# Kernel optimization log

Hardware: AMD Instinct MI355X
Metric: run time of the kernel (lower is better)

The kernel has to match this reference:

```python
import jax, jax.numpy as jnp
import numpy as np

N_NODES = 50000
N_EDGES = 1_600_000
IN_DIM = 6
EMB = 64
EDGE_DIM = 1
L = 4
BN_EPS = 1e-5


def _bn_relu(x, gamma, beta):
    # BatchNorm1d in training mode: biased batch stats over the row dim.
    mu = jnp.mean(x, axis=0)
    var = jnp.var(x, axis=0)
    xhat = (x - mu) * jax.lax.rsqrt(var + BN_EPS)
    return jax.nn.relu(xhat * gamma + beta)


def setup_inputs() -> dict:
    key = jax.random.key(0)
    ks = jax.random.split(key, 32)
    s = 0.1
    inp = {
        "x": jax.random.normal(ks[0], (N_NODES, IN_DIM), jnp.float32),
        "edge_index": jax.random.randint(ks[1], (2, N_EDGES), 0, N_NODES),
        "edge_attr": jax.random.normal(ks[2], (N_EDGES, EDGE_DIM), jnp.float32),
        "lin_in_W": jax.random.normal(ks[3], (IN_DIM, EMB)) * s,
        "lin_in_b": jnp.zeros((EMB,)),
        # per-layer stacked params, leading dim L
        "msg_W1": jax.random.normal(ks[4], (L, 2 * EMB + EDGE_DIM, EMB)) * s,
        "msg_b1": jnp.zeros((L, EMB)),
        "msg_g1": jnp.ones((L, EMB)),
        "msg_be1": jnp.zeros((L, EMB)),
        "msg_W2": jax.random.normal(ks[5], (L, EMB, EMB)) * s,
        "msg_b2": jnp.zeros((L, EMB)),
        "msg_g2": jnp.ones((L, EMB)),
        "msg_be2": jnp.zeros((L, EMB)),
        "upd_W1": jax.random.normal(ks[6], (L, 2 * EMB, EMB)) * s,
        "upd_b1": jnp.zeros((L, EMB)),
        "upd_g1": jnp.ones((L, EMB)),
        "upd_be1": jnp.zeros((L, EMB)),
        "upd_W2": jax.random.normal(ks[7], (L, EMB, EMB)) * s,
        "upd_b2": jnp.zeros((L, EMB)),
        "upd_g2": jnp.ones((L, EMB)),
        "upd_be2": jnp.zeros((L, EMB)),
        "pred_W": jax.random.normal(ks[8], (EMB, 1)) * s,
        "pred_b": jnp.zeros((1,)),
    }
    return inp


def reference(x, edge_index, edge_attr, lin_in_W, lin_in_b,
              msg_W1, msg_b1, msg_g1, msg_be1, msg_W2, msg_b2, msg_g2, msg_be2,
              upd_W1, upd_b1, upd_g1, upd_be1, upd_W2, upd_b2, upd_g2, upd_be2,
              pred_W, pred_b):
    n = x.shape[0]
    src = edge_index[0]  # j (source)
    dst = edge_index[1]  # i (target / aggregation index)

    h = x @ lin_in_W + lin_in_b  # (n, d)
    for l in range(L):
        h_i = h[dst]                              # (e, d) destination feats
        h_j = h[src]                              # (e, d) source feats
        m = jnp.concatenate([h_i, h_j, edge_attr], axis=-1)  # (e, 2d+de)
        m = _bn_relu(m @ msg_W1[l] + msg_b1[l], msg_g1[l], msg_be1[l])
        m = _bn_relu(m @ msg_W2[l] + msg_b2[l], msg_g2[l], msg_be2[l])
        aggr = jax.ops.segment_sum(m, dst, num_segments=n)   # (n, d)
        u = jnp.concatenate([h, aggr], axis=-1)              # (n, 2d)
        u = _bn_relu(u @ upd_W1[l] + upd_b1[l], upd_g1[l], upd_be1[l])
        u = _bn_relu(u @ upd_W2[l] + upd_b2[l], upd_g2[l], upd_be2[l])
        h = h + u  # residual
    out = h @ pred_W + pred_b
    return out.reshape(-1)
```

## Files before the change

### kernel.cpp

```cpp
#include <hip/hip_runtime.h>
#include <hip/hip_bf16.h>


#define BN_EPS 1e-5f
#define NSH 128
#define TPB 4
#define LYS 72
#define LW1S 168
#define LW2S 68
#define ASW 66

typedef __attribute__((ext_vector_type(4))) short short4v;
typedef __attribute__((ext_vector_type(8))) short short8;
typedef __attribute__((ext_vector_type(16))) float floatx16;

#define MFMA32 __builtin_amdgcn_mfma_f32_32x32x16_bf16

__device__ __forceinline__ short f2bs(float f) {
  union { float f; unsigned u; } x; x.f = f;
  unsigned r = x.u + 0x7fffu + ((x.u >> 16) & 1u);
  return (short)(r >> 16);
}
__device__ __forceinline__ short f2bs_fast(float f) {
  union { float f; unsigned u; } x; x.f = f;
  return (short)((x.u + 0x8000u) >> 16);
}
__device__ __forceinline__ float bs2f(short s) {
  union { unsigned u; float f; } x;
  x.u = ((unsigned)(unsigned short)s) << 16;
  return x.f;
}


__global__ void lin_in_kernel(const float* __restrict__ x,
                              const float* __restrict__ W,
                              const float* __restrict__ b, float* __restrict__ h,
                              short* __restrict__ hb, int N) {
  int gid = blockIdx.x * blockDim.x + threadIdx.x;
  if (gid >= N * 64) return;
  int n = gid >> 6, o = gid & 63;
  float acc = b[o];
#pragma unroll
  for (int k = 0; k < 6; ++k) acc += x[n * 6 + k] * W[k * 64 + o];
  h[gid] = acc;
  hb[gid] = f2bs(acc);
}

__global__ void deg_kernel(const int* __restrict__ ei, int* __restrict__ deg,
                           int E) {
  int gid = blockIdx.x * blockDim.x + threadIdx.x;
  if (gid < E) atomicAdd(&deg[ei[E + gid]], 1);
}

__global__ void scan_kernel(const int* __restrict__ deg, int* __restrict__ offs,
                            int N) {
  __shared__ int s[1024];
  int t = threadIdx.x;
  int chunk = (N + 1023) >> 10;
  int lo = t * chunk, hi = lo + chunk;
  if (hi > N) hi = N;
  if (lo > N) lo = N;
  int tot = 0;
  for (int i = lo; i < hi; ++i) tot += deg[i];
  s[t] = tot;
  __syncthreads();
  for (int off = 1; off < 1024; off <<= 1) {
    int v = (t >= off) ? s[t - off] : 0;
    __syncthreads();
    s[t] += v;
    __syncthreads();
  }
  int run = s[t] - tot;
  for (int i = lo; i < hi; ++i) {
    offs[i] = run;
    run += deg[i];
  }
}

__global__ void fill_kernel(const int* __restrict__ ei,
                            const int* __restrict__ offs, int* __restrict__ cnt,
                            int* __restrict__ sorted, int E) {
  int gid = blockIdx.x * blockDim.x + threadIdx.x;
  if (gid >= E) return;
  int d = ei[E + gid];
  int pos = offs[d] + atomicAdd(&cnt[d], 1);
  sorted[pos] = gid;
}

__global__ void gather_edges_kernel(const int* __restrict__ ei,
                                    const int* __restrict__ sorted,
                                    const float* __restrict__ ea,
                                    int* __restrict__ dd, int* __restrict__ ds,
                                    short* __restrict__ es, int E, int Epad) {
  int i = blockIdx.x * 256 + threadIdx.x;
  if (i >= Epad) return;
  if (i < E) {
    int e = sorted[i];
    dd[i] = ei[E + e];
    ds[i] = ei[e];
    es[i] = f2bs(ea[e]);
  } else {
    dd[i] = -1;
    ds[i] = 0;
    es[i] = 0;
  }
}

__global__ void pack_w1_kernel(const float* __restrict__ W,
                               short* __restrict__ Wt, int L_) {
  int i = blockIdx.x * 256 + threadIdx.x;
  if (i >= L_ * 64 * 160) return;
  int k = i % 160, n = (i / 160) % 64, l = i / (160 * 64);
  Wt[i] = (k < 129) ? f2bs(W[((size_t)l * 129 + k) * 64 + n]) : (short)0;
}

__global__ void pack_w2_kernel(const float* __restrict__ W,
                               short* __restrict__ Wt, int L_) {
  int i = blockIdx.x * 256 + threadIdx.x;
  if (i >= L_ * 64 * 64) return;
  int k = i % 64, n = (i / 64) % 64, l = i / 4096;
  Wt[i] = f2bs(W[((size_t)l * 64 + k) * 64 + n]);
}

__global__ void bn_finalize_kernel(const float* __restrict__ shards,
                                   const float* __restrict__ gamma,
                                   const float* __restrict__ beta, float cnt,
                                   float* __restrict__ ac) {
  int o = threadIdx.x;
  float s = 0.f, q = 0.f;
  for (int i = 0; i < NSH; ++i) {
    s += shards[i * 128 + o];
    q += shards[i * 128 + 64 + o];
  }
  float mu = s / cnt;
  float var = fmaxf(q / cnt - mu * mu, 0.f);
  float r = rsqrtf(var + BN_EPS);
  float g = gamma[o];
  ac[o] = g * r;
  ac[64 + o] = beta[o] - mu * g * r;
}

__global__ void bn_finalize_pack1(const float* __restrict__ shards,
                                  const float* __restrict__ gamma,
                                  const float* __restrict__ beta, float cnt,
                                  const float* __restrict__ W,
                                  const float* __restrict__ b,
                                  short* __restrict__ Wt,
                                  float* __restrict__ bs) {
  __shared__ float sa[64];
  int t = threadIdx.x;
  if (t < 64) {
    float s = 0.f, q = 0.f;
    for (int i = 0; i < NSH; ++i) {
      s += shards[i * 128 + t];
      q += shards[i * 128 + 64 + t];
    }
    float mu = s / cnt;
    float var = fmaxf(q / cnt - mu * mu, 0.f);
    float r = rsqrtf(var + BN_EPS);
    float a = gamma[t] * r;
    float c = beta[t] - mu * a;
    sa[t] = a;
    if (blockIdx.x == 0) bs[t] = a * b[t] + c;
  }
  __syncthreads();
  int i = blockIdx.x * 256 + t;
  if (i < 64 * 160) {
    int k = i % 160, n = i / 160;
    Wt[i] = (k < 129) ? f2bs(W[k * 64 + n] * sa[n]) : (short)0;
  }
}

__global__ void bn_finalize_pack2(const float* __restrict__ shards,
                                  const float* __restrict__ gamma,
                                  const float* __restrict__ beta, float cnt,
                                  const float* __restrict__ W,
                                  const float* __restrict__ b,
                                  short* __restrict__ Wt,
                                  float* __restrict__ bs) {
  __shared__ float sa[64];
  int t = threadIdx.x;
  if (t < 64) {
    float s = 0.f, q = 0.f;
    for (int i = 0; i < NSH; ++i) {
      s += shards[i * 128 + t];
      q += shards[i * 128 + 64 + t];
    }
    float mu = s / cnt;
    float var = fmaxf(q / cnt - mu * mu, 0.f);
    float r = rsqrtf(var + BN_EPS);
    float a = gamma[t] * r;
    float c = beta[t] - mu * a;
    sa[t] = a;
    if (blockIdx.x == 0) bs[t] = a * b[t] + c;
  }
  __syncthreads();
  int i = blockIdx.x * 256 + t;
  if (i < 64 * 64) {
    int k = i % 64, n = i / 64;
    Wt[i] = f2bs(W[k * 64 + n] * sa[n]);
  }
}


__device__ __forceinline__ void stage_w1(const short* __restrict__ Wt,
                                         short* Lw, int t) {
#pragma unroll
  for (int i = 0; i < 5; ++i) {
    int c = t + i * 256;
    int col = c / 20, ch = c % 20;
    *(short8*)&Lw[col * LW1S + ch * 8] = *(const short8*)&Wt[col * 160 + ch * 8];
  }
}
__device__ __forceinline__ void stage_w2(const short* __restrict__ Wt,
                                         short* Lw, int t) {
#pragma unroll
  for (int i = 0; i < 2; ++i) {
    int c = t + i * 256;
    int col = c >> 3, ch = c & 7;
    *(short8*)&Lw[col * LW2S + ch * 8] = *(const short8*)&Wt[col * 64 + ch * 8];
  }
}

__device__ __forceinline__ void gemm1_32(const short* __restrict__ hbf,
                                         const short* Lw1,
                                         const float* __restrict__ bias, int d,
                                         int sx, short eav, int me, int hl,
                                         floatx16 acc[2]) {
  const short* hd = hbf + (size_t)d * 64 + hl * 8;
  const short* hs = hbf + (size_t)sx * 64 + hl * 8;
  short8 A[8];
#pragma unroll
  for (int kc = 0; kc < 4; ++kc) A[kc] = *(const short8*)(hd + kc * 16);
#pragma unroll
  for (int kc = 0; kc < 4; ++kc) A[4 + kc] = *(const short8*)(hs + kc * 16);
  short8 a8 = {0, 0, 0, 0, 0, 0, 0, 0};
  if (hl == 0) a8[0] = eav;
#pragma unroll
  for (int nt = 0; nt < 2; ++nt) {
    int col = nt * 32 + me;
    float bv = bias[col];
    floatx16 a;
#pragma unroll
    for (int r = 0; r < 16; ++r) a[r] = bv;
    const short* wp = Lw1 + col * LW1S + hl * 8;
#pragma unroll
    for (int kc = 0; kc < 8; ++kc) {
      short8 B = *(const short8*)(wp + kc * 16);
      a = MFMA32(A[kc], B, a, 0, 0, 0);
    }
    short8 B8 = *(const short8*)(wp + 128);
    a = MFMA32(a8, B8, a, 0, 0, 0);
    acc[nt] = a;
  }
}

__device__ __forceinline__ void load_frag(const short* __restrict__ hbf, int d,
                                          int sx, int hl, short8 Bf[8]) {
  int dc = d < 0 ? 0 : d;
  const short* hd = hbf + (size_t)dc * 64 + hl * 8;
  const short* hs = hbf + (size_t)sx * 64 + hl * 8;
#pragma unroll
  for (int kc = 0; kc < 4; ++kc) Bf[kc] = *(const short8*)(hd + kc * 16);
#pragma unroll
  for (int kc = 0; kc < 4; ++kc) Bf[4 + kc] = *(const short8*)(hs + kc * 16);
}

__device__ __forceinline__ void gemm1T_mfma(const short* Lw1,
                                            const short8 Bf[8], short eav,
                                            int me, int hl, floatx16 acc[2]) {
  short8 b8 = {0, 0, 0, 0, 0, 0, 0, 0};
  if (hl == 0) b8[0] = eav;
#pragma unroll
  for (int nt = 0; nt < 2; ++nt) {
    floatx16 a;
#pragma unroll
    for (int r = 0; r < 16; ++r) a[r] = 0.f;
    const short* wp = Lw1 + (nt * 32 + me) * LW1S + hl * 8;
#pragma unroll
    for (int kc = 0; kc < 8; ++kc) {
      short8 A = *(const short8*)(wp + kc * 16);
      a = MFMA32(A, Bf[kc], a, 0, 0, 0);
    }
    short8 A8 = *(const short8*)(wp + 128);
    a = MFMA32(A8, b8, a, 0, 0, 0);
    acc[nt] = a;
  }
}

__device__ __forceinline__ void gemm1T_32(const short* __restrict__ hbf,
                                          const short* Lw1, int d, int sx,
                                          short eav, int me, int hl,
                                          floatx16 acc[2]) {
  short8 Bf[8];
  load_frag(hbf, d, sx, hl, Bf);
  gemm1T_mfma(Lw1, Bf, eav, me, hl, acc);
}

__device__ __forceinline__ void write_z(short* Lz, const floatx16 acc[2],
                                        const float b1v[2][16], int w, int me,
                                        int hl) {
#pragma unroll
  for (int nt = 0; nt < 2; ++nt)
#pragma unroll
    for (int g4 = 0; g4 < 4; ++g4) {
      int n1b = nt * 32 + 8 * g4 + 4 * hl;
      short4v pk;
#pragma unroll
      for (int j = 0; j < 4; ++j) {
        int r = g4 * 4 + j;
        pk[j] = f2bs_fast(fmaxf(acc[nt][r] + b1v[nt][r], 0.f));
      }
      *(short4v*)&Lz[(w * 32 + me) * LYS + n1b] = pk;
    }
}

__device__ __forceinline__ void gemm2_32(const short* Lz, const short* Lw2,
                                         const float* __restrict__ bias, int w,
                                         int me, int hl, floatx16 acc[2]) {
  short8 Z[4];
  const short* zp = &Lz[(w * 32 + me) * LYS + hl * 8];
#pragma unroll
  for (int kc = 0; kc < 4; ++kc) Z[kc] = *(const short8*)(zp + kc * 16);
#pragma unroll
  for (int nt = 0; nt < 2; ++nt) {
    int col = nt * 32 + me;
    float bv = bias[col];
    floatx16 a;
#pragma unroll
    for (int r = 0; r < 16; ++r) a[r] = bv;
    const short* wp = Lw2 + col * LW2S + hl * 8;
#pragma unroll
    for (int kc = 0; kc < 4; ++kc) {
      short8 B = *(const short8*)(wp + kc * 16);
      a = MFMA32(Z[kc], B, a, 0, 0, 0);
    }
    acc[nt] = a;
  }
}

__device__ __forceinline__ void stats32_acc(const floatx16 acc[2], int idx0,
                                            int w, int hl, int E, bool full,
                                            float sa[2], float qa[2]) {
#pragma unroll
  for (int nt = 0; nt < 2; ++nt) {
    float s = 0.f, q = 0.f;
#pragma unroll
    for (int r = 0; r < 16; ++r) {
      float v = acc[nt][r];
      if (!full) {
        int row = (r & 3) + 8 * (r >> 2) + 4 * hl;
        if (idx0 + w * 32 + row >= E) v = 0.f;
      }
      s += v;
      q += v * v;
    }
    s += __shfl_down(s, 32, 64);
    q += __shfl_down(q, 32, 64);
    sa[nt] += s;
    qa[nt] += q;
  }
}

__device__ __forceinline__ void stats_epilogue(float sred[4][128],
                                               const float sa[2],
                                               const float qa[2], int w,
                                               int lane, int t,
                                               float* __restrict__ stat,
                                               int shard) {
  if (lane < 32) {
#pragma unroll
    for (int nt = 0; nt < 2; ++nt) {
      sred[w][nt * 32 + lane] = sa[nt];
      sred[w][64 + nt * 32 + lane] = qa[nt];
    }
  }
  __syncthreads();
  if (t < 128) {
    float v = sred[0][t] + sred[1][t] + sred[2][t] + sred[3][t];
    atomicAdd(&stat[(size_t)shard * 128 + t], v);
  }
}


__global__ __launch_bounds__(256) void edge_pass_a(
    const short* __restrict__ hbf, const short* __restrict__ Wt1,
    const float* __restrict__ b1, const int* __restrict__ dd,
    const int* __restrict__ dsr, const short* __restrict__ es,
    float* __restrict__ stat, int E, int Epad) {
  __shared__ __align__(16) short Lw1[64 * LW1S];
  __shared__ float sred[4][128];
  int t = threadIdx.x;
  stage_w1(Wt1, Lw1, t);
  __syncthreads();
  int w = t >> 6, lane = t & 63, me = lane & 31, hl = lane >> 5;
  float sa[2] = {0.f, 0.f}, qa[2] = {0.f, 0.f};
  for (int it = 0; it < TPB; ++it) {
    int idx0 = (blockIdx.x * TPB + it) * 128;
    if (idx0 >= Epad) break;
    int eg = idx0 + w * 32 + me;
    int d = dd[eg];
    int dc = d < 0 ? 0 : d;
    int sx = dsr[eg];
    short eav = es[eg];
    floatx16 acc[2];
    gemm1_32(hbf, Lw1, b1, dc, sx, eav, me, hl, acc);
    stats32_acc(acc, idx0, w, hl, E, idx0 + 128 <= E, sa, qa);
  }
  stats_epilogue(sred, sa, qa, w, lane, t, stat, blockIdx.x & (NSH - 1));
}

__global__ __launch_bounds__(256) void edge_pass_b(
    const short* __restrict__ hbf, const short* __restrict__ Wt1s,
    const float* __restrict__ b1s, const int* __restrict__ dd,
    const int* __restrict__ dsr, const short* __restrict__ es,
    const short* __restrict__ Wt2, const float* __restrict__ b2,
    float* __restrict__ stat, int E, int Epad) {
  __shared__ __align__(16) short Lw1[64 * LW1S];
  __shared__ __align__(16) short Lw2[64 * LW2S];
  __shared__ __align__(16) short Lz[128 * LYS];
  __shared__ float sred[4][128];
  int t = threadIdx.x;
  stage_w1(Wt1s, Lw1, t);
  stage_w2(Wt2, Lw2, t);
  __syncthreads();
  int w = t >> 6, lane = t & 63, me = lane & 31, hl = lane >> 5;
  float b1v[2][16];
#pragma unroll
  for (int nt = 0; nt < 2; ++nt)
#pragma unroll
    for (int r = 0; r < 16; ++r)
      b1v[nt][r] = b1s[nt * 32 + (r & 3) + 8 * (r >> 2) + 4 * hl];
  float sa[2] = {0.f, 0.f}, qa[2] = {0.f, 0.f};
  for (int it = 0; it < TPB; ++it) {
    int idx0 = (blockIdx.x * TPB + it) * 128;
    if (idx0 >= Epad) break;
    int eg = idx0 + w * 32 + me;
    int d = dd[eg];
    int dc = d < 0 ? 0 : d;
    int sx = dsr[eg];
    short eav = es[eg];
    floatx16 acc[2];
    gemm1T_32(hbf, Lw1, dc, sx, eav, me, hl, acc);
    write_z(Lz, acc, b1v, w, me, hl);
    floatx16 acc2[2];
    gemm2_32(Lz, Lw2, b2, w, me, hl, acc2);
    stats32_acc(acc2, idx0, w, hl, E, idx0 + 128 <= E, sa, qa);
  }
  stats_epilogue(sred, sa, qa, w, lane, t, stat, blockIdx.x & (NSH - 1));
}

__global__ __launch_bounds__(256) void edge_pass_c(
    const short* __restrict__ hbf, const short* __restrict__ Wt1s,
    const float* __restrict__ b1s, const int* __restrict__ dd,
    const int* __restrict__ dsr, const short* __restrict__ es,
    const short* __restrict__ Wt2s, const float* __restrict__ b2s,
    float* __restrict__ aggr, int E, int Epad) {
  __shared__ __align__(16) short Lw1[64 * LW1S];
  __shared__ __align__(16) short Lw2[64 * LW2S];
  __shared__ __align__(16) short Lz[128 * LYS];
  __shared__ int sdstw[4][32];
  int t = threadIdx.x;
  stage_w1(Wt1s, Lw1, t);
  stage_w2(Wt2s, Lw2, t);
  int w = t >> 6, lane = t & 63, me = lane & 31, hl = lane >> 5;
  const int base0 = blockIdx.x * TPB * 128;
  int d_c, sx_c, d_n, sx_n;
  short eav_c, eav_n;
  {
    int eg = base0 + w * 32 + me;
    d_c = dd[eg];
    sx_c = dsr[eg];
    eav_c = es[eg];
    int i1 = base0 + 128;
    if (i1 < Epad) {
      d_n = dd[i1 + w * 32 + me];
      sx_n = dsr[i1 + w * 32 + me];
      eav_n = es[i1 + w * 32 + me];
    } else {
      d_n = -1;
      sx_n = 0;
      eav_n = 0;
    }
  }
  short8 Bf_c[8], Bf_n[8];
  load_frag(hbf, d_c, sx_c, hl, Bf_c);
  __syncthreads();
  float b1v[2][16];
#pragma unroll
  for (int nt = 0; nt < 2; ++nt)
#pragma unroll
    for (int r = 0; r < 16; ++r)
      b1v[nt][r] = b1s[nt * 32 + (r & 3) + 8 * (r >> 2) + 4 * hl];
#pragma unroll
  for (int it = 0; it < TPB; ++it) {
    int idx0 = base0 + it * 128;
    if (idx0 < Epad) {
      bool nv = (idx0 + 128) < Epad;
      if (nv) load_frag(hbf, d_n, sx_n, hl, Bf_n);
      int d_2 = -1, sx_2 = 0;
      short eav_2 = 0;
      int i2 = idx0 + 256;
      if (it + 2 < TPB && i2 < Epad) {
        d_2 = dd[i2 + w * 32 + me];
        sx_2 = dsr[i2 + w * 32 + me];
        eav_2 = es[i2 + w * 32 + me];
      }
      if (lane < 32) sdstw[w][lane] = d_c;
      floatx16 acc[2];
      gemm1T_mfma(Lw1, Bf_c, eav_c, me, hl, acc);
      write_z(Lz, acc, b1v, w, me, hl);
      floatx16 acc2[2];
      gemm2_32(Lz, Lw2, b2s, w, me, hl, acc2);
      float s0 = 0.f, s1 = 0.f;
      int d2 = sdstw[w][4 * hl];
#pragma unroll
      for (int g4 = 0; g4 < 4; ++g4) {
#pragma unroll
        for (int j = 0; j < 4; ++j) {
          int r = g4 * 4 + j;
          s0 += fmaxf(acc2[0][r], 0.f);
          s1 += fmaxf(acc2[1][r], 0.f);
          int offn;
          if (j == 3)
            offn = (g4 == 3) ? -1 : 8 * (g4 + 1) + 4 * hl;
          else
            offn = 8 * g4 + 4 * hl + j + 1;
          int dn = (offn < 0) ? -2 : sdstw[w][offn];
          if (d2 != dn) {
            if (d2 >= 0) {
              atomicAdd(&aggr[(size_t)d2 * 64 + me], s0);
              atomicAdd(&aggr[(size_t)d2 * 64 + me + 32], s1);
            }
            s0 = 0.f;
            s1 = 0.f;
          }
          d2 = dn;
        }
      }
#pragma unroll
      for (int kc = 0; kc < 8; ++kc) Bf_c[kc] = Bf_n[kc];
      d_c = d_n;
      sx_c = sx_n;
      eav_c = eav_n;
      d_n = d_2;
      sx_n = sx_2;
      eav_n = eav_2;
    }
  }
}


__device__ __forceinline__ void gemm_r2c8(const float* __restrict__ As,
                                          const float* __restrict__ W, int K,
                                          int rg, int cg, float acc[2][8]) {
  const float* ap = As + rg * 2;
  const float* wp = W + cg * 8;
#pragma unroll 4
  for (int k = 0; k < K; ++k) {
    float2 a = *(const float2*)&ap[k * ASW];
    float4 w0 = *(const float4*)&wp[k * 64];
    float4 w1 = *(const float4*)&wp[k * 64 + 4];
    float wv[8] = {w0.x, w0.y, w0.z, w0.w, w1.x, w1.y, w1.z, w1.w};
#pragma unroll
    for (int j = 0; j < 8; ++j) {
      acc[0][j] += a.x * wv[j];
      acc[1][j] += a.y * wv[j];
    }
  }
}

__device__ __forceinline__ void stats_r2c8(const float acc[2][8],
                                           float* __restrict__ shard, int t,
                                           int cg) {
  float s[8], q[8];
#pragma unroll
  for (int j = 0; j < 8; ++j) {
    s[j] = acc[0][j] + acc[1][j];
    q[j] = acc[0][j] * acc[0][j] + acc[1][j] * acc[1][j];
  }
#pragma unroll
  for (int off = 32; off >= 8; off >>= 1) {
#pragma unroll
    for (int j = 0; j < 8; ++j) {
      s[j] += __shfl_down(s[j], off, 64);
      q[j] += __shfl_down(q[j], off, 64);
    }
  }
  if (((t & 63) >> 3) == 0) {
#pragma unroll
    for (int j = 0; j < 8; ++j) {
      atomicAdd(&shard[cg * 8 + j], s[j]);
      atomicAdd(&shard[64 + cg * 8 + j], q[j]);
    }
  }
}

__global__ __launch_bounds__(256) void node_gemm1_v3(
    const float* __restrict__ h, const float* __restrict__ aggr,
    const float* __restrict__ W, const float* __restrict__ b,
    float* __restrict__ u1, float* __restrict__ stat, int N) {
  __shared__ __align__(16) float As[128 * ASW];
  int n0 = blockIdx.x * 64;
  int t = threadIdx.x;
  int c = t & 63, g = t >> 6;
  for (int n = g; n < 64; n += 4) {
    int idx = n0 + n;
    bool v = idx < N;
    As[c * ASW + n] = v ? h[(size_t)idx * 64 + c] : 0.f;
    As[(64 + c) * ASW + n] = v ? aggr[(size_t)idx * 64 + c] : 0.f;
  }
  __syncthreads();
  int rg = t >> 3, cg = t & 7;
  float acc[2][8];
#pragma unroll
  for (int i = 0; i < 2; ++i)
#pragma unroll
    for (int j = 0; j < 8; ++j) acc[i][j] = b[cg * 8 + j];
  gemm_r2c8(As, W, 128, rg, cg, acc);
#pragma unroll
  for (int i = 0; i < 2; ++i) {
    int idx = n0 + rg * 2 + i;
    if (idx < N) {
      *(float4*)&u1[(size_t)idx * 64 + cg * 8] =
          make_float4(acc[i][0], acc[i][1], acc[i][2], acc[i][3]);
      *(float4*)&u1[(size_t)idx * 64 + cg * 8 + 4] =
          make_float4(acc[i][4], acc[i][5], acc[i][6], acc[i][7]);
    } else {
#pragma unroll
      for (int j = 0; j < 8; ++j) acc[i][j] = 0.f;
    }
  }
  stats_r2c8(acc, stat + (size_t)(blockIdx.x & (NSH - 1)) * 128, t, cg);
}

__global__ __launch_bounds__(256) void node_gemm2_v3(
    const float* __restrict__ u1, const float* __restrict__ ac,
    const float* __restrict__ W, const float* __restrict__ b,
    float* __restrict__ u2, float* __restrict__ stat, int N) {
  __shared__ __align__(16) float As[64 * ASW];
  int n0 = blockIdx.x * 64;
  int t = threadIdx.x;
  int c = t & 63, g = t >> 6;
  float a1 = ac[c], c1 = ac[64 + c];
  for (int n = g; n < 64; n += 4) {
    int idx = n0 + n;
    bool v = idx < N;
    As[c * ASW + n] = v ? fmaxf(u1[(size_t)idx * 64 + c] * a1 + c1, 0.f) : 0.f;
  }
  __syncthreads();
  int rg = t >> 3, cg = t & 7;
  float acc[2][8];
#pragma unroll
  for (int i = 0; i < 2; ++i)
#pragma unroll
    for (int j = 0; j < 8; ++j) acc[i][j] = b[cg * 8 + j];
  gemm_r2c8(As, W, 64, rg, cg, acc);
#pragma unroll
  for (int i = 0; i < 2; ++i) {
    int idx = n0 + rg * 2 + i;
    if (idx < N) {
      *(float4*)&u2[(size_t)idx * 64 + cg * 8] =
          make_float4(acc[i][0], acc[i][1], acc[i][2], acc[i][3]);
      *(float4*)&u2[(size_t)idx * 64 + cg * 8 + 4] =
          make_float4(acc[i][4], acc[i][5], acc[i][6], acc[i][7]);
    } else {
#pragma unroll
      for (int j = 0; j < 8; ++j) acc[i][j] = 0.f;
    }
  }
  stats_r2c8(acc, stat + (size_t)(blockIdx.x & (NSH - 1)) * 128, t, cg);
}

__global__ void residual_kernel(float* __restrict__ h, short* __restrict__ hb,
                                const float* __restrict__ u2,
                                const float* __restrict__ ac, int total) {
  int gid = blockIdx.x * blockDim.x + threadIdx.x;
  if (gid >= total) return;
  int o = gid & 63;
  float v = u2[gid] * ac[o] + ac[64 + o];
  float nv = h[gid] + fmaxf(v, 0.f);
  h[gid] = nv;
  hb[gid] = f2bs(nv);
}

__global__ void pred_kernel(const float* __restrict__ h,
                            const float* __restrict__ W,
                            const float* __restrict__ b,
                            float* __restrict__ out, int N) {
  int n = blockIdx.x * blockDim.x + threadIdx.x;
  if (n >= N) return;
  float acc = b[0];
  const float* hr = h + (size_t)n * 64;
#pragma unroll
  for (int o = 0; o < 64; ++o) acc += hr[o] * W[o];
  out[n] = acc;
}


extern "C" void kernel_launch(void* const* d_in, const int* in_sizes, int n_in,
                              void* d_out, int out_size, void* d_ws,
                              size_t ws_size, hipStream_t stream) {
  const float* x = (const float*)d_in[0];
  const int* ei = (const int*)d_in[1];
  const float* ea = (const float*)d_in[2];
  const float* lin_W = (const float*)d_in[3];
  const float* lin_b = (const float*)d_in[4];
  const float* msg_W1 = (const float*)d_in[5];
  const float* msg_b1 = (const float*)d_in[6];
  const float* msg_g1 = (const float*)d_in[7];
  const float* msg_be1 = (const float*)d_in[8];
  const float* msg_W2 = (const float*)d_in[9];
  const float* msg_b2 = (const float*)d_in[10];
  const float* msg_g2 = (const float*)d_in[11];
  const float* msg_be2 = (const float*)d_in[12];
  const float* upd_W1 = (const float*)d_in[13];
  const float* upd_b1 = (const float*)d_in[14];
  const float* upd_g1 = (const float*)d_in[15];
  const float* upd_be1 = (const float*)d_in[16];
  const float* upd_W2 = (const float*)d_in[17];
  const float* upd_b2 = (const float*)d_in[18];
  const float* upd_g2 = (const float*)d_in[19];
  const float* upd_be2 = (const float*)d_in[20];
  const float* pred_W = (const float*)d_in[21];
  const float* pred_b = (const float*)d_in[22];
  float* out = (float*)d_out;

  const int N = in_sizes[0] / 6;
  const int E = in_sizes[1] / 2;
  const int L = 4;
  const int Epad = ((E + 127) / 128) * 128;

  char* p = (char*)d_ws;
  auto alloc = [&](size_t bytes) {
    void* r = (void*)p;
    p += (bytes + 255) & ~(size_t)255;
    return r;
  };
  float* h = (float*)alloc((size_t)N * 64 * 4);
  short* hb = (short*)alloc((size_t)N * 64 * 2);
  float* aggr = (float*)alloc((size_t)N * 64 * 4);
  float* stats = (float*)alloc((size_t)4 * NSH * 128 * 4);
  float* acu1 = (float*)alloc(128 * 4);
  float* acu2 = (float*)alloc(128 * 4);
  float* b1s = (float*)alloc(64 * 4);
  float* b2s = (float*)alloc(64 * 4);
  float* u1 = (float*)alloc((size_t)N * 64 * 4);
  float* u2 = (float*)alloc((size_t)N * 64 * 4);
  int* deg = (int*)alloc((size_t)N * 4);
  int* offs = (int*)alloc((size_t)N * 4);
  int* cnt = (int*)alloc((size_t)N * 4);
  int* sorted = (int*)alloc((size_t)E * 4);
  int* dd = (int*)alloc((size_t)Epad * 4);
  int* dsr = (int*)alloc((size_t)Epad * 4);
  short* es = (short*)alloc((size_t)Epad * 2);
  short* Wt1 = (short*)alloc((size_t)L * 64 * 160 * 2);
  short* Wt2 = (short*)alloc((size_t)L * 64 * 64 * 2);
  short* Wt1s = (short*)alloc((size_t)64 * 160 * 2);
  short* Wt2s = (short*)alloc((size_t)64 * 64 * 2);

  const int B = 256;
  const size_t REG = (size_t)NSH * 128;
  int gridE256 = (E + 255) / 256;
  int NT = Epad / 128;
  int gridEdge = (NT + TPB - 1) / TPB;
  int gridM64 = (N + 63) / 64;
  int gridN64 = (N * 64 + B - 1) / B;
  int gridN = (N + B - 1) / B;

  hipMemsetAsync(deg, 0, (size_t)N * 4, stream);
  hipMemsetAsync(cnt, 0, (size_t)N * 4, stream);
  lin_in_kernel<<<gridN64, B, 0, stream>>>(x, lin_W, lin_b, h, hb, N);
  deg_kernel<<<gridE256, B, 0, stream>>>(ei, deg, E);
  scan_kernel<<<1, 1024, 0, stream>>>(deg, offs, N);
  fill_kernel<<<gridE256, B, 0, stream>>>(ei, offs, cnt, sorted, E);
  gather_edges_kernel<<<(Epad + 255) / 256, B, 0, stream>>>(ei, sorted, ea, dd,
                                                            dsr, es, E, Epad);
  pack_w1_kernel<<<(L * 64 * 160 + 255) / 256, B, 0, stream>>>(msg_W1, Wt1, L);
  pack_w2_kernel<<<(L * 64 * 64 + 255) / 256, B, 0, stream>>>(msg_W2, Wt2, L);

  for (int l = 0; l < L; ++l) {
    const short* Wt1l = Wt1 + (size_t)l * 64 * 160;
    const short* Wt2l = Wt2 + (size_t)l * 64 * 64;
    const float* U1 = upd_W1 + (size_t)l * 128 * 64;
    const float* U2 = upd_W2 + (size_t)l * 64 * 64;
    hipMemsetAsync(aggr, 0, (size_t)N * 64 * 4 + (size_t)4 * REG * 4, stream);
    edge_pass_a<<<gridEdge, 256, 0, stream>>>(hb, Wt1l, msg_b1 + l * 64, dd,
                                              dsr, es, stats, E, Epad);
    bn_finalize_pack1<<<(64 * 160 + 255) / 256, B, 0, stream>>>(
        stats, msg_g1 + l * 64, msg_be1 + l * 64, (float)E,
        msg_W1 + (size_t)l * 129 * 64, msg_b1 + l * 64, Wt1s, b1s);
    edge_pass_b<<<gridEdge, 256, 0, stream>>>(hb, Wt1s, b1s, dd, dsr, es, Wt2l,
                                              msg_b2 + l * 64, stats + REG, E,
                                              Epad);
    bn_finalize_pack2<<<(64 * 64 + 255) / 256, B, 0, stream>>>(
        stats + REG, msg_g2 + l * 64, msg_be2 + l * 64, (float)E,
        msg_W2 + (size_t)l * 64 * 64, msg_b2 + l * 64, Wt2s, b2s);
    edge_pass_c<<<gridEdge, 256, 0, stream>>>(hb, Wt1s, b1s, dd, dsr, es, Wt2s,
                                              b2s, aggr, E, Epad);
    node_gemm1_v3<<<gridM64, 256, 0, stream>>>(h, aggr, U1, upd_b1 + l * 64,
                                               u1, stats + 2 * REG, N);
    bn_finalize_kernel<<<1, 64, 0, stream>>>(stats + 2 * REG, upd_g1 + l * 64,
                                             upd_be1 + l * 64, (float)N, acu1);
    node_gemm2_v3<<<gridM64, 256, 0, stream>>>(u1, acu1, U2, upd_b2 + l * 64,
                                               u2, stats + 3 * REG, N);
    bn_finalize_kernel<<<1, 64, 0, stream>>>(stats + 3 * REG, upd_g2 + l * 64,
                                             upd_be2 + l * 64, (float)N, acu2);
    residual_kernel<<<gridN64, B, 0, stream>>>(h, hb, u2, acu2, N * 64);
  }
  pred_kernel<<<gridN, B, 0, stream>>>(h, pred_W, pred_b, out, N);
}
```

Baseline: 1.870 ms.

## Software-pipeline edge gathers in BN stats passes with register double-buffering

The two edge passes that compute batch-norm statistics now prefetch the next tile's gathered node features and the tile-after-next's edge indices into registers while the current tile's MFMAs run. The first tile's loads are issued before the weight-staging barrier, so global gather latency overlaps with LDS staging and compute. The cost is roughly double the fragment registers per thread (two sets of eight short8 fragments), which may lower occupancy. A fully unrolled loop replaces the early break.

```diff
diff --git a/kernel.cpp b/kernel.cpp
--- a/kernel.cpp
+++ b/kernel.cpp
@@ -222,39 +222,6 @@
   }
 }
 
-__device__ __forceinline__ void gemm1_32(const short* __restrict__ hbf,
-                                         const short* Lw1,
-                                         const float* __restrict__ bias, int d,
-                                         int sx, short eav, int me, int hl,
-                                         floatx16 acc[2]) {
-  const short* hd = hbf + (size_t)d * 64 + hl * 8;
-  const short* hs = hbf + (size_t)sx * 64 + hl * 8;
-  short8 A[8];
-#pragma unroll
-  for (int kc = 0; kc < 4; ++kc) A[kc] = *(const short8*)(hd + kc * 16);
-#pragma unroll
-  for (int kc = 0; kc < 4; ++kc) A[4 + kc] = *(const short8*)(hs + kc * 16);
-  short8 a8 = {0, 0, 0, 0, 0, 0, 0, 0};
-  if (hl == 0) a8[0] = eav;
-#pragma unroll
-  for (int nt = 0; nt < 2; ++nt) {
-    int col = nt * 32 + me;
-    float bv = bias[col];
-    floatx16 a;
-#pragma unroll
-    for (int r = 0; r < 16; ++r) a[r] = bv;
-    const short* wp = Lw1 + col * LW1S + hl * 8;
-#pragma unroll
-    for (int kc = 0; kc < 8; ++kc) {
-      short8 B = *(const short8*)(wp + kc * 16);
-      a = MFMA32(A[kc], B, a, 0, 0, 0);
-    }
-    short8 B8 = *(const short8*)(wp + 128);
-    a = MFMA32(a8, B8, a, 0, 0, 0);
-    acc[nt] = a;
-  }
-}
-
 __device__ __forceinline__ void load_frag(const short* __restrict__ hbf, int d,
                                           int sx, int hl, short8 Bf[8]) {
   int dc = d < 0 ? 0 : d;
@@ -266,6 +233,32 @@
   for (int kc = 0; kc < 4; ++kc) Bf[4 + kc] = *(const short8*)(hs + kc * 16);
 }
 
+__device__ __forceinline__ void gemm1_mfma_std(const short* Lw1,
+                                               const float* __restrict__ bias,
+                                               const short8 Af[8], short eav,
+                                               int me, int hl,
+                                               floatx16 acc[2]) {
+  short8 a8 = {0, 0, 0, 0, 0, 0, 0, 0};
+  if (hl == 0) a8[0] = eav;
+#pragma unroll
+  for (int nt = 0; nt < 2; ++nt) {
+    int col = nt * 32 + me;
+    float bv = bias[col];
+    floatx16 a;
+#pragma unroll
+    for (int r = 0; r < 16; ++r) a[r] = bv;
+    const short* wp = Lw1 + col * LW1S + hl * 8;
+#pragma unroll
+    for (int kc = 0; kc < 8; ++kc) {
+      short8 B = *(const short8*)(wp + kc * 16);
+      a = MFMA32(Af[kc], B, a, 0, 0, 0);
+    }
+    short8 B8 = *(const short8*)(wp + 128);
+    a = MFMA32(a8, B8, a, 0, 0, 0);
+    acc[nt] = a;
+  }
+}
+
 __device__ __forceinline__ void gemm1T_mfma(const short* Lw1,
                                             const short8 Bf[8], short eav,
                                             int me, int hl, floatx16 acc[2]) {
@@ -286,15 +279,6 @@
     a = MFMA32(A8, b8, a, 0, 0, 0);
     acc[nt] = a;
   }
-}
-
-__device__ __forceinline__ void gemm1T_32(const short* __restrict__ hbf,
-                                          const short* Lw1, int d, int sx,
-                                          short eav, int me, int hl,
-                                          floatx16 acc[2]) {
-  short8 Bf[8];
-  load_frag(hbf, d, sx, hl, Bf);
-  gemm1T_mfma(Lw1, Bf, eav, me, hl, acc);
 }
 
 __device__ __forceinline__ void write_z(short* Lz, const floatx16 acc[2],
@@ -392,20 +376,56 @@
   __shared__ float sred[4][128];
   int t = threadIdx.x;
   stage_w1(Wt1, Lw1, t);
+  int w = t >> 6, lane = t & 63, me = lane & 31, hl = lane >> 5;
+  const int base0 = blockIdx.x * TPB * 128;
+  int d_c, sx_c, d_n, sx_n;
+  short eav_c, eav_n;
+  {
+    int eg = base0 + w * 32 + me;
+    d_c = dd[eg];
+    sx_c = dsr[eg];
+    eav_c = es[eg];
+    int i1 = base0 + 128;
+    if (i1 < Epad) {
+      d_n = dd[i1 + w * 32 + me];
+      sx_n = dsr[i1 + w * 32 + me];
+      eav_n = es[i1 + w * 32 + me];
+    } else {
+      d_n = -1;
+      sx_n = 0;
+      eav_n = 0;
+    }
+  }
+  short8 Af_c[8], Af_n[8];
+  load_frag(hbf, d_c, sx_c, hl, Af_c);
   __syncthreads();
-  int w = t >> 6, lane = t & 63, me = lane & 31, hl = lane >> 5;
   float sa[2] = {0.f, 0.f}, qa[2] = {0.f, 0.f};
+#pragma unroll
   for (int it = 0; it < TPB; ++it) {
-    int idx0 = (blockIdx.x * TPB + it) * 128;
-    if (idx0 >= Epad) break;
-    int eg = idx0 + w * 32 + me;
-    int d = dd[eg];
-    int dc = d < 0 ? 0 : d;
-    int sx = dsr[eg];
-    short eav = es[eg];
-    floatx16 acc[2];
-    gemm1_32(hbf, Lw1, b1, dc, sx, eav, me, hl, acc);
-    stats32_acc(acc, idx0, w, hl, E, idx0 + 128 <= E, sa, qa);
+    int idx0 = base0 + it * 128;
+    if (idx0 < Epad) {
+      bool nv = (idx0 + 128) < Epad;
+      if (nv) load_frag(hbf, d_n, sx_n, hl, Af_n);
+      int d_2 = -1, sx_2 = 0;
+      short eav_2 = 0;
+      int i2 = idx0 + 256;
+      if (it + 2 < TPB && i2 < Epad) {
+        d_2 = dd[i2 + w * 32 + me];
+        sx_2 = dsr[i2 + w * 32 + me];
+        eav_2 = es[i2 + w * 32 + me];
+      }
+      floatx16 acc[2];
+      gemm1_mfma_std(Lw1, b1, Af_c, eav_c, me, hl, acc);
+      stats32_acc(acc, idx0, w, hl, E, idx0 + 128 <= E, sa, qa);
+#pragma unroll
+      for (int kc = 0; kc < 8; ++kc) Af_c[kc] = Af_n[kc];
+      d_c = d_n;
+      sx_c = sx_n;
+      eav_c = eav_n;
+      d_n = d_2;
+      sx_n = sx_2;
+      eav_n = eav_2;
+    }
   }
   stats_epilogue(sred, sa, qa, w, lane, t, stat, blockIdx.x & (NSH - 1));
 }
@@ -423,8 +443,29 @@
   int t = threadIdx.x;
   stage_w1(Wt1s, Lw1, t);
   stage_w2(Wt2, Lw2, t);
+  int w = t >> 6, lane = t & 63, me = lane & 31, hl = lane >> 5;
+  const int base0 = blockIdx.x * TPB * 128;
+  int d_c, sx_c, d_n, sx_n;
+  short eav_c, eav_n;
+  {
+    int eg = base0 + w * 32 + me;
+    d_c = dd[eg];
+    sx_c = dsr[eg];
+    eav_c = es[eg];
+    int i1 = base0 + 128;
+    if (i1 < Epad) {
+      d_n = dd[i1 + w * 32 + me];
+      sx_n = dsr[i1 + w * 32 + me];
+      eav_n = es[i1 + w * 32 + me];
+    } else {
+      d_n = -1;
+      sx_n = 0;
+      eav_n = 0;
+    }
+  }
+  short8 Bf_c[8], Bf_n[8];
+  load_frag(hbf, d_c, sx_c, hl, Bf_c);
   __syncthreads();
-  int w = t >> 6, lane = t & 63, me = lane & 31, hl = lane >> 5;
   float b1v[2][16];
 #pragma unroll
   for (int nt = 0; nt < 2; ++nt)
@@ -432,20 +473,35 @@
     for (int r = 0; r < 16; ++r)
       b1v[nt][r] = b1s[nt * 32 + (r & 3) + 8 * (r >> 2) + 4 * hl];
   float sa[2] = {0.f, 0.f}, qa[2] = {0.f, 0.f};
+#pragma unroll
   for (int it = 0; it < TPB; ++it) {
-    int idx0 = (blockIdx.x * TPB + it) * 128;
-    if (idx0 >= Epad) break;
-    int eg = idx0 + w * 32 + me;
-    int d = dd[eg];
-    int dc = d < 0 ? 0 : d;
-    int sx = dsr[eg];
-    short eav = es[eg];
-    floatx16 acc[2];
-    gemm1T_32(hbf, Lw1, dc, sx, eav, me, hl, acc);
-    write_z(Lz, acc, b1v, w, me, hl);
-    floatx16 acc2[2];
-    gemm2_32(Lz, Lw2, b2, w, me, hl, acc2);
-    stats32_acc(acc2, idx0, w, hl, E, idx0 + 128 <= E, sa, qa);
+    int idx0 = base0 + it * 128;
+    if (idx0 < Epad) {
+      bool nv = (idx0 + 128) < Epad;
+      if (nv) load_frag(hbf, d_n, sx_n, hl, Bf_n);
+      int d_2 = -1, sx_2 = 0;
+      short eav_2 = 0;
+      int i2 = idx0 + 256;
+      if (it + 2 < TPB && i2 < Epad) {
+        d_2 = dd[i2 + w * 32 + me];
+        sx_2 = dsr[i2 + w * 32 + me];
+        eav_2 = es[i2 + w * 32 + me];
+      }
+      floatx16 acc[2];
+      gemm1T_mfma(Lw1, Bf_c, eav_c, me, hl, acc);
+      write_z(Lz, acc, b1v, w, me, hl);
+      floatx16 acc2[2];
+      gemm2_32(Lz, Lw2, b2, w, me, hl, acc2);
+      stats32_acc(acc2, idx0, w, hl, E, idx0 + 128 <= E, sa, qa);
+#pragma unroll
+      for (int kc = 0; kc < 8; ++kc) Bf_c[kc] = Bf_n[kc];
+      d_c = d_n;
+      sx_c = sx_n;
+      eav_c = eav_n;
+      d_n = d_2;
+      sx_n = sx_2;
+      eav_n = eav_2;
+    }
   }
   stats_epilogue(sred, sa, qa, w, lane, t, stat, blockIdx.x & (NSH - 1));
 }
```

Result: slower. 1.946 ms (+4.1%).

## Hold second-layer weights in registers and move bias to LDS for occupancy

Applied to the files above, without the earlier changes.

Layer-2 message weights now stay in per-lane registers instead of an LDS tile. The first-layer bias, formerly a 32-float register array per thread, now lives in a small LDS array read as float4. The stats reduction reuses the Lz buffer instead of a separate shared array. Launch bounds request 4 blocks per CU. The aim is to free LDS and VGPRs for higher occupancy in the edge passes, at the cost of more register pressure from the weight fragments and extra LDS reads for the bias.

```diff
diff --git a/kernel.cpp b/kernel.cpp
--- a/kernel.cpp
+++ b/kernel.cpp
@@ -7,7 +7,6 @@
 #define TPB 4
 #define LYS 72
 #define LW1S 168
-#define LW2S 68
 #define ASW 66
 
 typedef __attribute__((ext_vector_type(4))) short short4v;
@@ -212,14 +211,34 @@
     *(short8*)&Lw[col * LW1S + ch * 8] = *(const short8*)&Wt[col * 160 + ch * 8];
   }
 }
-__device__ __forceinline__ void stage_w2(const short* __restrict__ Wt,
-                                         short* Lw, int t) {
-#pragma unroll
-  for (int i = 0; i < 2; ++i) {
-    int c = t + i * 256;
-    int col = c >> 3, ch = c & 7;
-    *(short8*)&Lw[col * LW2S + ch * 8] = *(const short8*)&Wt[col * 64 + ch * 8];
-  }
+
+__device__ __forceinline__ void stage_b1l(const float* __restrict__ b1s,
+                                          float* Lb1, int t) {
+  if (t < 64) {
+    int hl_ = t >> 5, rem = t & 31, nt_ = rem >> 4, r_ = rem & 15;
+    Lb1[t] = b1s[nt_ * 32 + (r_ & 3) + 8 * (r_ >> 2) + 4 * hl_];
+  }
+}
+
+__device__ __forceinline__ void load_w2_regs(const short* __restrict__ Wt2,
+                                             int me, int hl, short8 w2r[2][4]) {
+#pragma unroll
+  for (int nt = 0; nt < 2; ++nt) {
+    const short* wp = Wt2 + (nt * 32 + me) * 64 + hl * 8;
+#pragma unroll
+    for (int kc = 0; kc < 4; ++kc) w2r[nt][kc] = *(const short8*)(wp + kc * 16);
+  }
+}
+
+__device__ __forceinline__ void load_frag(const short* __restrict__ hbf, int d,
+                                          int sx, int hl, short8 Bf[8]) {
+  int dc = d < 0 ? 0 : d;
+  const short* hd = hbf + (size_t)dc * 64 + hl * 8;
+  const short* hs = hbf + (size_t)sx * 64 + hl * 8;
+#pragma unroll
+  for (int kc = 0; kc < 4; ++kc) Bf[kc] = *(const short8*)(hd + kc * 16);
+#pragma unroll
+  for (int kc = 0; kc < 4; ++kc) Bf[4 + kc] = *(const short8*)(hs + kc * 16);
 }
 
 __device__ __forceinline__ void gemm1_32(const short* __restrict__ hbf,
@@ -255,17 +274,6 @@
   }
 }
 
-__device__ __forceinline__ void load_frag(const short* __restrict__ hbf, int d,
-                                          int sx, int hl, short8 Bf[8]) {
-  int dc = d < 0 ? 0 : d;
-  const short* hd = hbf + (size_t)dc * 64 + hl * 8;
-  const short* hs = hbf + (size_t)sx * 64 + hl * 8;
-#pragma unroll
-  for (int kc = 0; kc < 4; ++kc) Bf[kc] = *(const short8*)(hd + kc * 16);
-#pragma unroll
-  for (int kc = 0; kc < 4; ++kc) Bf[4 + kc] = *(const short8*)(hs + kc * 16);
-}
-
 __device__ __forceinline__ void gemm1T_mfma(const short* Lw1,
                                             const short8 Bf[8], short eav,
                                             int me, int hl, floatx16 acc[2]) {
@@ -298,43 +306,38 @@
 }
 
 __device__ __forceinline__ void write_z(short* Lz, const floatx16 acc[2],
-                                        const float b1v[2][16], int w, int me,
+                                        const float* Lb1, int w, int me,
                                         int hl) {
 #pragma unroll
   for (int nt = 0; nt < 2; ++nt)
 #pragma unroll
     for (int g4 = 0; g4 < 4; ++g4) {
+      float4 bq = *(const float4*)&Lb1[hl * 32 + nt * 16 + 4 * g4];
       int n1b = nt * 32 + 8 * g4 + 4 * hl;
       short4v pk;
-#pragma unroll
-      for (int j = 0; j < 4; ++j) {
-        int r = g4 * 4 + j;
-        pk[j] = f2bs_fast(fmaxf(acc[nt][r] + b1v[nt][r], 0.f));
-      }
+      pk[0] = f2bs_fast(fmaxf(acc[nt][4 * g4 + 0] + bq.x, 0.f));
+      pk[1] = f2bs_fast(fmaxf(acc[nt][4 * g4 + 1] + bq.y, 0.f));
+      pk[2] = f2bs_fast(fmaxf(acc[nt][4 * g4 + 2] + bq.z, 0.f));
+      pk[3] = f2bs_fast(fmaxf(acc[nt][4 * g4 + 3] + bq.w, 0.f));
       *(short4v*)&Lz[(w * 32 + me) * LYS + n1b] = pk;
     }
 }
 
-__device__ __forceinline__ void gemm2_32(const short* Lz, const short* Lw2,
-                                         const float* __restrict__ bias, int w,
-                                         int me, int hl, floatx16 acc[2]) {
+__device__ __forceinline__ void gemm2_w2r(const short* Lz,
+                                          const short8 w2r[2][4],
+                                          const float bv2[2], int w, int me,
+                                          int hl, floatx16 acc[2]) {
   short8 Z[4];
   const short* zp = &Lz[(w * 32 + me) * LYS + hl * 8];
 #pragma unroll
   for (int kc = 0; kc < 4; ++kc) Z[kc] = *(const short8*)(zp + kc * 16);
 #pragma unroll
   for (int nt = 0; nt < 2; ++nt) {
-    int col = nt * 32 + me;
-    float bv = bias[col];
     floatx16 a;
 #pragma unroll
-    for (int r = 0; r < 16; ++r) a[r] = bv;
-    const short* wp = Lw2 + col * LW2S + hl * 8;
-#pragma unroll
-    for (int kc = 0; kc < 4; ++kc) {
-      short8 B = *(const short8*)(wp + kc * 16);
-      a = MFMA32(Z[kc], B, a, 0, 0, 0);
-    }
+    for (int r = 0; r < 16; ++r) a[r] = bv2[nt];
+#pragma unroll
+    for (int kc = 0; kc < 4; ++kc) a = MFMA32(Z[kc], w2r[nt][kc], a, 0, 0, 0);
     acc[nt] = a;
   }
 }
@@ -378,6 +381,28 @@
   __syncthreads();
   if (t < 128) {
     float v = sred[0][t] + sred[1][t] + sred[2][t] + sred[3][t];
+    atomicAdd(&stat[(size_t)shard * 128 + t], v);
+  }
+}
+
+__device__ __forceinline__ void stats_epilogue_lz(short* Lz, const float sa[2],
+                                                  const float qa[2], int w,
+                                                  int lane, int t,
+                                                  float* __restrict__ stat,
+                                                  int shard) {
+  float* sw = (float*)&Lz[(w * 32) * LYS];
+  if (lane < 32) {
+#pragma unroll
+    for (int nt = 0; nt < 2; ++nt) {
+      sw[nt * 32 + lane] = sa[nt];
+      sw[64 + nt * 32 + lane] = qa[nt];
+    }
+  }
+  __syncthreads();
+  if (t < 128) {
+    float v = 0.f;
+#pragma unroll
+    for (int wq = 0; wq < 4; ++wq) v += ((float*)&Lz[(wq * 32) * LYS])[t];
     atomicAdd(&stat[(size_t)shard * 128 + t], v);
   }
 }
@@ -410,27 +435,23 @@
   stats_epilogue(sred, sa, qa, w, lane, t, stat, blockIdx.x & (NSH - 1));
 }
 
-__global__ __launch_bounds__(256) void edge_pass_b(
+__global__ __launch_bounds__(256, 4) void edge_pass_b(
     const short* __restrict__ hbf, const short* __restrict__ Wt1s,
     const float* __restrict__ b1s, const int* __restrict__ dd,
     const int* __restrict__ dsr, const short* __restrict__ es,
     const short* __restrict__ Wt2, const float* __restrict__ b2,
     float* __restrict__ stat, int E, int Epad) {
   __shared__ __align__(16) short Lw1[64 * LW1S];
-  __shared__ __align__(16) short Lw2[64 * LW2S];
   __shared__ __align__(16) short Lz[128 * LYS];
-  __shared__ float sred[4][128];
+  __shared__ __align__(16) float Lb1[64];
   int t = threadIdx.x;
+  int w = t >> 6, lane = t & 63, me = lane & 31, hl = lane >> 5;
   stage_w1(Wt1s, Lw1, t);
-  stage_w2(Wt2, Lw2, t);
-  __syncthreads();
-  int w = t >> 6, lane = t & 63, me = lane & 31, hl = lane >> 5;
-  float b1v[2][16];
-#pragma unroll
-  for (int nt = 0; nt < 2; ++nt)
-#pragma unroll
-    for (int r = 0; r < 16; ++r)
-      b1v[nt][r] = b1s[nt * 32 + (r & 3) + 8 * (r >> 2) + 4 * hl];
+  stage_b1l(b1s, Lb1, t);
+  short8 w2r[2][4];
+  load_w2_regs(Wt2, me, hl, w2r);
+  float bv2[2] = {b2[me], b2[32 + me]};
+  __syncthreads();
   float sa[2] = {0.f, 0.f}, qa[2] = {0.f, 0.f};
   for (int it = 0; it < TPB; ++it) {
     int idx0 = (blockIdx.x * TPB + it) * 128;
@@ -442,28 +463,31 @@
     short eav = es[eg];
     floatx16 acc[2];
     gemm1T_32(hbf, Lw1, dc, sx, eav, me, hl, acc);
-    write_z(Lz, acc, b1v, w, me, hl);
+    write_z(Lz, acc, Lb1, w, me, hl);
     floatx16 acc2[2];
-    gemm2_32(Lz, Lw2, b2, w, me, hl, acc2);
+    gemm2_w2r(Lz, w2r, bv2, w, me, hl, acc2);
     stats32_acc(acc2, idx0, w, hl, E, idx0 + 128 <= E, sa, qa);
   }
-  stats_epilogue(sred, sa, qa, w, lane, t, stat, blockIdx.x & (NSH - 1));
-}
-
-__global__ __launch_bounds__(256) void edge_pass_c(
+  stats_epilogue_lz(Lz, sa, qa, w, lane, t, stat, blockIdx.x & (NSH - 1));
+}
+
+__global__ __launch_bounds__(256, 4) void edge_pass_c(
     const short* __restrict__ hbf, const short* __restrict__ Wt1s,
     const float* __restrict__ b1s, const int* __restrict__ dd,
     const int* __restrict__ dsr, const short* __restrict__ es,
     const short* __restrict__ Wt2s, const float* __restrict__ b2s,
     float* __restrict__ aggr, int E, int Epad) {
   __shared__ __align__(16) short Lw1[64 * LW1S];
-  __shared__ __align__(16) short Lw2[64 * LW2S];
   __shared__ __align__(16) short Lz[128 * LYS];
+  __shared__ __align__(16) float Lb1[64];
   __shared__ int sdstw[4][32];
   int t = threadIdx.x;
+  int w = t >> 6, lane = t & 63, me = lane & 31, hl = lane >> 5;
   stage_w1(Wt1s, Lw1, t);
-  stage_w2(Wt2s, Lw2, t);
-  int w = t >> 6, lane = t & 63, me = lane & 31, hl = lane >> 5;
+  stage_b1l(b1s, Lb1, t);
+  short8 w2r[2][4];
+  load_w2_regs(Wt2s, me, hl, w2r);
+  float bv2[2] = {b2s[me], b2s[32 + me]};
   const int base0 = blockIdx.x * TPB * 128;
   int d_c, sx_c, d_n, sx_n;
   short eav_c, eav_n;
@@ -486,12 +510,6 @@
   short8 Bf_c[8], Bf_n[8];
   load_frag(hbf, d_c, sx_c, hl, Bf_c);
   __syncthreads();
-  float b1v[2][16];
-#pragma unroll
-  for (int nt = 0; nt < 2; ++nt)
-#pragma unroll
-    for (int r = 0; r < 16; ++r)
-      b1v[nt][r] = b1s[nt * 32 + (r & 3) + 8 * (r >> 2) + 4 * hl];
 #pragma unroll
   for (int it = 0; it < TPB; ++it) {
     int idx0 = base0 + it * 128;
@@ -509,9 +527,9 @@
       if (lane < 32) sdstw[w][lane] = d_c;
       floatx16 acc[2];
       gemm1T_mfma(Lw1, Bf_c, eav_c, me, hl, acc);
-      write_z(Lz, acc, b1v, w, me, hl);
+      write_z(Lz, acc, Lb1, w, me, hl);
       floatx16 acc2[2];
-      gemm2_32(Lz, Lw2, b2s, w, me, hl, acc2);
+      gemm2_w2r(Lz, w2r, bv2, w, me, hl, acc2);
       float s0 = 0.f, s1 = 0.f;
       int d2 = sdstw[w][4 * hl];
 #pragma unroll
```

Measured after the change: 2.262 ms. +21.0%, slower.
